# Performance work log

Hardware: AMD Instinct MI355X
Metric: run time of the kernel (lower is better)

The kernel has to match this reference:

```python
import jax, jax.numpy as jnp
import numpy as np

DIM, H, W, DEPTH = 256, 64, 64, 4
D_STATE, DT_RANK, D_CONV = 8, 16, 4
G, AGENTS = 8, 4

PKEYS = ['ln_w','ln_b','in_proj_w','conv_w','conv_b','x_proj_w','dt_proj_w','dt_proj_b',
         'A_log','A_b_log','D','out_proj_w','mn_w','mn_b']


def layernorm(x, w, b, eps=1e-5):
    mu = jnp.mean(x, -1, keepdims=True)
    var = jnp.var(x, -1, keepdims=True)
    return (x - mu) * jax.lax.rsqrt(var + eps) * w + b


def causal_conv1d(x, w, b):
    # x: (g, d, L); w: (d, k) depthwise causal conv (pad left k-1)
    k = w.shape[-1]
    xp = jnp.pad(x, ((0, 0), (0, 0), (k - 1, 0)))
    y = jax.lax.conv_general_dilated(xp, w[:, None, :], (1,), 'VALID',
                                     dimension_numbers=('NCH', 'OIH', 'NCH'),
                                     feature_group_count=w.shape[0])
    return y + b[None, :, None]


def selective_scan(u, delta, A, B, C, Dp, z):
    # u, delta, z: (g, d, L); B, C: (g, n, L); A: (d, n); Dp: (d,)
    dT = jnp.moveaxis(delta, -1, 0)
    BT = jnp.moveaxis(B, -1, 0)
    CT = jnp.moveaxis(C, -1, 0)
    uT = jnp.moveaxis(u, -1, 0)
    h0 = jnp.zeros(u.shape[:2] + (A.shape[-1],), u.dtype)  # (g, d, n)

    def step(h, inp):
        d_t, B_t, C_t, u_t = inp  # (g,d),(g,n),(g,n),(g,d)
        h = jnp.exp(d_t[..., None] * A) * h + (d_t * u_t)[..., None] * B_t[:, None, :]
        return h, jnp.einsum('gdn,gn->gd', h, C_t)

    _, ys = jax.lax.scan(step, h0, (dT, BT, CT, uT))
    y = jnp.moveaxis(ys, 0, -1) + Dp[None, :, None] * u
    return y * jax.nn.silu(z)


def ssm_dir(xdl, zdl, p, A):
    # one scan direction of mamba_inner_fn_no_out_proj; xdl, zdl: (g, d, L)
    xc = jax.nn.silu(causal_conv1d(xdl, p['conv_w'], p['conv_b']))
    x_dbl = jnp.einsum('gdl,ed->gel', xc, p['x_proj_w'])  # e = dt_rank + 2n
    dt, B, C = jnp.split(x_dbl, [DT_RANK, DT_RANK + D_STATE], axis=1)
    delta = jax.nn.softplus(jnp.einsum('grl,dr->gdl', dt, p['dt_proj_w'])
                            + p['dt_proj_b'][None, :, None])
    return selective_scan(xc, delta, A, B, C, p['D'], zdl)


def single_mamba_block(x, p):
    # x: (g, L, c)  -- LayerNorm + bidirectional Mamba (bimamba v1) + residual
    skip = x
    xn = layernorm(x, p['ln_w'], p['ln_b'])
    xz = jnp.einsum('glc,ec->gle', xn, p['in_proj_w'])  # (g, L, 2d), no bias
    xx, z = jnp.split(xz, 2, axis=-1)
    xdl = jnp.swapaxes(xx, 1, 2)
    zdl = jnp.swapaxes(z, 1, 2)
    y_f = ssm_dir(xdl, zdl, p, -jnp.exp(p['A_log']))
    y_b = jnp.flip(ssm_dir(jnp.flip(xdl, -1), jnp.flip(zdl, -1), p, -jnp.exp(p['A_b_log'])), -1)
    y = 0.5 * (y_f + y_b)  # if_devide_out=True
    out = jnp.einsum('gdl,od->glo', y, p['out_proj_w'])  # no bias
    out = layernorm(out, p['mn_w'], p['mn_b'])  # use_norm=True
    return out + skip


def _forward(data, plist, record_len):
    b, c, h, w = data.shape
    rl = np.asarray(record_len)
    seg = jnp.asarray(np.repeat(np.arange(rl.shape[0]), rl))
    means = jax.ops.segment_sum(data, seg, num_segments=rl.shape[0]) \
        / jnp.asarray(rl, data.dtype)[:, None, None, None]
    x = means.reshape(rl.shape[0], c, h * w).transpose(0, 2, 1)  # (G, L, C)
    for i in range(DEPTH):
        p = {k: v[i] for k, v in zip(PKEYS, plist)}
        x = single_mamba_block(x, p)
    return x.transpose(0, 2, 1).reshape(rl.shape[0], c, h, w)


def setup_inputs() -> dict:
    key = jax.random.key(0)
    ks = jax.random.split(key, 8)
    nrm = lambda k, shape, sc: jax.random.normal(k, shape, jnp.float32) * sc
    Alog = jnp.zeros((DEPTH, DIM, D_STATE), jnp.float32) \
        + jnp.log(jnp.arange(1, D_STATE + 1, dtype=jnp.float32))
    return {
        'data': jax.random.normal(ks[0], (G * AGENTS, DIM, H, W), jnp.float32),
        'ln_w': jnp.ones((DEPTH, DIM)), 'ln_b': jnp.zeros((DEPTH, DIM)),
        'in_proj_w': nrm(ks[1], (DEPTH, 2 * DIM, DIM), 0.02),
        'conv_w': nrm(ks[2], (DEPTH, DIM, D_CONV), 0.3),
        'conv_b': jnp.zeros((DEPTH, DIM)),
        'x_proj_w': nrm(ks[3], (DEPTH, DT_RANK + 2 * D_STATE, DIM), 0.02),
        'dt_proj_w': nrm(ks[4], (DEPTH, DIM, DT_RANK), 0.1),
        'dt_proj_b': jnp.full((DEPTH, DIM), float(np.log(np.expm1(0.01))), jnp.float32),
        'A_log': Alog, 'A_b_log': Alog,
        'D': jnp.ones((DEPTH, DIM)),
        'out_proj_w': nrm(ks[5], (DEPTH, DIM, DIM), 0.02),
        'mn_w': jnp.ones((DEPTH, DIM)), 'mn_b': jnp.zeros((DEPTH, DIM)),
        'record_len': jnp.full((G,), AGENTS, dtype=jnp.int32),
    }


def reference(data, ln_w, ln_b, in_proj_w, conv_w, conv_b, x_proj_w, dt_proj_w, dt_proj_b,
              A_log, A_b_log, D, out_proj_w, mn_w, mn_b, record_len):
    plist = [ln_w, ln_b, in_proj_w, conv_w, conv_b, x_proj_w, dt_proj_w, dt_proj_b,
             A_log, A_b_log, D, out_proj_w, mn_w, mn_b]
    return _forward(data, plist, record_len)
```

## Files before the change

### kernel.cpp

```cpp
#include <hip/hip_runtime.h>
#include <hip/hip_bf16.h>
#include <cstdint>
#include <cstddef>

typedef unsigned short u16;
typedef unsigned int   u32;

typedef short s16x8 __attribute__((ext_vector_type(8)));
typedef float f32x4 __attribute__((ext_vector_type(4)));

__device__ __forceinline__ float b2f(u16 u){ u32 x = ((u32)u)<<16; float f; __builtin_memcpy(&f,&x,4); return f; }
__device__ __forceinline__ u16  f2b(float f){ u32 x; __builtin_memcpy(&x,&f,4); u32 r = x + 0x7FFFu + ((x>>16)&1u); return (u16)(r>>16); }

__device__ __forceinline__ void unpack8(uint4 v, float* o){
  o[0]=b2f((u16)v.x); o[1]=b2f((u16)(v.x>>16));
  o[2]=b2f((u16)v.y); o[3]=b2f((u16)(v.y>>16));
  o[4]=b2f((u16)v.z); o[5]=b2f((u16)(v.z>>16));
  o[6]=b2f((u16)v.w); o[7]=b2f((u16)(v.w>>16));
}

__device__ __forceinline__ void gl_lds16(const u16* g, u16* l){
  __builtin_amdgcn_global_load_lds((const __attribute__((address_space(1))) u32*)g,
                                   (__attribute__((address_space(3))) u32*)l, 16, 0, 0);
}

__global__ void k_detect(const u16* __restrict__ lnw, int* __restrict__ flag){
  if (threadIdx.x==0 && blockIdx.x==0) *flag = (lnw[0] == 0x3F80) ? 1 : 0;
}

struct CvtTable { const void* src[14]; u16* dst[14]; int n[14]; };
__global__ void k_cvt(CvtTable t, const int* __restrict__ flag){
  int ti = blockIdx.y;
  int n = t.n[ti];
  int isbf = *flag;
  const u16*  sb = (const u16*)t.src[ti];
  const float* sf = (const float*)t.src[ti];
  u16* d = t.dst[ti];
  for (int i = blockIdx.x*256 + threadIdx.x; i < n; i += gridDim.x*256)
    d[i] = isbf ? sb[i] : f2b(sf[i]);
}

__global__ void k_mean(const void* __restrict__ data, const int* __restrict__ rl,
                       float* __restrict__ x, const int* __restrict__ flag){
  __shared__ float tile[32][129];
  int isbf = *flag;
  const u16*  db = (const u16*)data;
  const float* df_ = (const float*)data;
  int g = blockIdx.z, c0 = blockIdx.y*32, l0 = blockIdx.x*128;
  int tid = threadIdx.x;
  int off=0; for(int i=0;i<g;i++) off += rl[i];
  int cnt = rl[g];
  float inv = 1.0f/(float)cnt;
  for(int it=0; it<16; ++it){
    int idx = it*256 + tid;
    int ci = idx>>7, lj = idx&127;
    float acc = 0.f;
    for(int b=0;b<cnt;b++){
      size_t gi = ((size_t)(off+b)*256 + (c0+ci)) * 4096 + (l0+lj);
      acc += isbf ? b2f(db[gi]) : df_[gi];
    }
    tile[ci][lj] = acc*inv;
  }
  __syncthreads();
  for(int it=0; it<16; ++it){
    int idx = it*256 + tid;
    int lj = idx>>5, ci = idx&31;
    x[ ((size_t)g*4096 + (l0+lj))*256 + (c0+ci) ] = tile[ci][lj];
  }
}

__global__ void k_prep(const u16* __restrict__ dtp, const u16* __restrict__ xpw, u16* __restrict__ bcomb){
  int layer = blockIdx.y, row = blockIdx.x, c = threadIdx.x;
  u16 out;
  if (row < 256){
    float acc = 0.f;
    #pragma unroll
    for(int r=0;r<16;r++)
      acc += b2f(dtp[(size_t)layer*4096 + row*16 + r]) * b2f(xpw[(size_t)layer*8192 + r*256 + c]);
    out = f2b(acc);
  } else if (row < 272){
    out = xpw[(size_t)layer*8192 + (16 + row - 256)*256 + c];
  } else {
    out = 0;
  }
  bcomb[((size_t)layer*384 + row)*256 + c] = out;
}

__global__ void k_ln1(const float* __restrict__ x, u16* __restrict__ xn,
                      const u16* __restrict__ w, const u16* __restrict__ b, int layer){
  int wid = threadIdx.x>>6, lane = threadIdx.x&63;
  int row = blockIdx.x*4 + wid;
  const float* xr = x + (size_t)row*256;
  float4 v = *(const float4*)(xr + lane*4);
  float s = v.x+v.y+v.z+v.w;
  float q = v.x*v.x+v.y*v.y+v.z*v.z+v.w*v.w;
  for(int o=32;o;o>>=1){ s += __shfl_xor(s,o); q += __shfl_xor(q,o); }
  float mu = s*(1.f/256.f);
  float var = q*(1.f/256.f) - mu*mu;
  float rs = rsqrtf(var + 1e-5f);
  const u16* wp = w + layer*256 + lane*4;
  const u16* bp = b + layer*256 + lane*4;
  float vv[4] = {v.x,v.y,v.z,v.w};
  u16 o4[4];
  #pragma unroll
  for(int k2=0;k2<4;k2++) o4[k2] = f2b( (vv[k2]-mu)*rs*b2f(wp[k2]) + b2f(bp[k2]) );
  uint2 ov; ov.x = (u32)o4[0] | ((u32)o4[1]<<16); ov.y = (u32)o4[2] | ((u32)o4[3]<<16);
  *(uint2*)(xn + (size_t)row*256 + lane*4) = ov;
}

template<int MODE>
__global__ __launch_bounds__(256)
void k_gemm(const u16* __restrict__ A, const u16* __restrict__ B,
            u16* __restrict__ C0, int ldC,
            const u16* __restrict__ bias, u16* __restrict__ C1){
  __shared__ u16 As[128*64];
  __shared__ u16 Bs[128*64];
  int tid = threadIdx.x, wid = tid>>6, lane = tid&63;
  int m0 = blockIdx.x*128, n0 = blockIdx.y*128;
  f32x4 acc[4][4];
  #pragma unroll
  for(int i=0;i<4;i++)
    #pragma unroll
    for(int j=0;j<4;j++) acc[i][j] = (f32x4){0.f,0.f,0.f,0.f};
  int lrow  = lane>>3;
  int scol  = ((lane&7) ^ lrow) * 8;
  int rm = (wid&1)*64, cn = (wid>>1)*64;
  for(int k0=0;k0<256;k0+=64){
    #pragma unroll
    for(int it=0; it<4; ++it){
      int chunk = wid*4 + it;
      int row = chunk*8 + lrow;
      gl_lds16(A + (size_t)(m0+row)*256 + k0 + scol, As + chunk*512 + lane*8);
      gl_lds16(B + (size_t)(n0+row)*256 + k0 + scol, Bs + chunk*512 + lane*8);
    }
    __syncthreads();
    #pragma unroll
    for(int kk=0;kk<2;kk++){
      s16x8 af[4], bfr[4];
      #pragma unroll
      for(int i=0;i<4;i++){
        int ar = rm + i*16 + (lane&15);
        int ap = (kk*4 + (lane>>4)) ^ (ar&7);
        af[i]  = *(const s16x8*)(As + ar*64 + ap*8);
        int br = cn + i*16 + (lane&15);
        int bp = (kk*4 + (lane>>4)) ^ (br&7);
        bfr[i] = *(const s16x8*)(Bs + br*64 + bp*8);
      }
      #pragma unroll
      for(int i=0;i<4;i++)
        #pragma unroll
        for(int j=0;j<4;j++)
          acc[i][j] = __builtin_amdgcn_mfma_f32_16x16x32_bf16(af[i], bfr[j], acc[i][j], 0,0,0);
    }
    __syncthreads();
  }
  #pragma unroll
  for(int i=0;i<4;i++){
    #pragma unroll
    for(int j=0;j<4;j++){
      int n  = n0 + cn + j*16 + (lane&15);
      int mB = m0 + rm + i*16 + ((lane>>4)<<2);
      #pragma unroll
      for(int r=0;r<4;r++){
        float val = acc[i][j][r];
        int m = mB + r;
        if (MODE==0){
          C0[(size_t)m*ldC + n] = f2b(val);
        } else {
          if (n < 256){
            float v2 = val + b2f(bias[n]);
            float sp = (v2 > 15.f) ? v2 : __logf(1.f + __expf(v2));
            C0[(size_t)m*256 + n] = f2b(sp);
          } else if (n < 272){
            C1[(size_t)m*16 + (n-256)] = f2b(val);
          }
        }
      }
    }
  }
}

__global__ void k_conv(const u16* __restrict__ xz, const u16* __restrict__ cw,
                       const u16* __restrict__ cb, u16* __restrict__ xcf, u16* __restrict__ xcb_, int layer){
  int l0 = blockIdx.x*4, g = blockIdx.y, d = threadIdx.x;
  float w[4];
  #pragma unroll
  for(int j=0;j<4;j++) w[j] = b2f(cw[(size_t)layer*1024 + d*4 + j]);
  float bb = b2f(cb[layer*256 + d]);
  float xv[10];
  #pragma unroll
  for(int t=0;t<10;t++){
    int lp = l0 - 3 + t;
    xv[t] = (lp>=0 && lp<4096) ? b2f(xz[((size_t)g*4096 + lp)*512 + d]) : 0.f;
  }
  #pragma unroll
  for(int i=0;i<4;i++){
    float af = bb, ab = bb;
    #pragma unroll
    for(int j=0;j<4;j++){ af += w[j]*xv[i+j]; ab += w[j]*xv[i+6-j]; }
    af = af / (1.f + __expf(-af));
    ab = ab / (1.f + __expf(-ab));
    size_t o = ((size_t)g*4096 + (l0+i))*256 + d;
    xcf[o]  = f2b(af);
    xcb_[o] = f2b(ab);
  }
}

__global__ __launch_bounds__(256)
void k_scan1(const u16* __restrict__ df, const u16* __restrict__ db,
             const u16* __restrict__ uf, const u16* __restrict__ ub,
             const u16* __restrict__ bcf, const u16* __restrict__ bcb,
             const u16* __restrict__ Alog, const u16* __restrict__ Ablog,
             float* __restrict__ abuf, float* __restrict__ bbuf, int layer){
  int c = blockIdx.x, g = blockIdx.y, dir = blockIdx.z, d = threadIdx.x;
  const u16* dl = dir ? db : df;
  const u16* uu = dir ? ub : uf;
  const u16* bc = dir ? bcb : bcf;
  const u16* Al = dir ? Ablog : Alog;
  float An[8], h[8], ap[8];
  #pragma unroll
  for(int n=0;n<8;n++){
    An[n] = -__expf(b2f(Al[(size_t)layer*2048 + d*8 + n]));
    h[n] = 0.f; ap[n] = 1.f;
  }
  #pragma unroll 4
  for(int t=0;t<64;t++){
    int ts = c*64 + t;
    int tg = dir ? (4095 - ts) : ts;
    size_t rowo = (size_t)g*4096 + tg;
    float dv = b2f(dl[rowo*256 + d]);
    float uv = b2f(uu[rowo*256 + d]);
    uint4 bv = *(const uint4*)(bc + rowo*16);
    float bn[8]; unpack8(bv, bn);
    float du = dv*uv;
    #pragma unroll
    for(int n=0;n<8;n++){
      float da = __expf(dv*An[n]);
      h[n] = fmaf(da, h[n], du*bn[n]);
      ap[n] *= da;
    }
  }
  size_t base = ((((size_t)dir*8+g)*64 + c)*256 + d)*8;
  *(float4*)(abuf+base)   = (float4){ap[0],ap[1],ap[2],ap[3]};
  *(float4*)(abuf+base+4) = (float4){ap[4],ap[5],ap[6],ap[7]};
  *(float4*)(bbuf+base)   = (float4){h[0],h[1],h[2],h[3]};
  *(float4*)(bbuf+base+4) = (float4){h[4],h[5],h[6],h[7]};
}

__global__ void k_scan2(const float* __restrict__ abuf, const float* __restrict__ bbuf,
                        float* __restrict__ hs){
  int dblk = blockIdx.x, g = blockIdx.y, dir = blockIdx.z;
  int n = threadIdx.x & 7, dd = threadIdx.x >> 3;
  int d = dblk*32 + dd;
  float h = 0.f;
  size_t gofs = (((size_t)dir*8+g)*64);
  for(int c=0;c<64;c++){
    size_t idx = ((gofs + c)*256 + d)*8 + n;
    hs[idx] = h;
    h = fmaf(abuf[idx], h, bbuf[idx]);
  }
}

__global__ __launch_bounds__(256)
void k_scan3(const u16* __restrict__ df, const u16* __restrict__ db,
             const u16* __restrict__ uf, const u16* __restrict__ ub,
             const u16* __restrict__ bcf, const u16* __restrict__ bcb,
             const u16* __restrict__ Alog, const u16* __restrict__ Ablog,
             const u16* __restrict__ Dp, const u16* __restrict__ xz,
             const float* __restrict__ hs,
             u16* __restrict__ yf, u16* __restrict__ yb, int layer){
  int c = blockIdx.x, g = blockIdx.y, dir = blockIdx.z, d = threadIdx.x;
  const u16* dl = dir ? db : df;
  const u16* uu = dir ? ub : uf;
  const u16* bc = dir ? bcb : bcf;
  const u16* Al = dir ? Ablog : Alog;
  u16* yo = dir ? yb : yf;
  float An[8], h[8];
  size_t base = ((((size_t)dir*8+g)*64 + c)*256 + d)*8;
  float4 h0 = *(const float4*)(hs+base);
  float4 h1 = *(const float4*)(hs+base+4);
  h[0]=h0.x; h[1]=h0.y; h[2]=h0.z; h[3]=h0.w;
  h[4]=h1.x; h[5]=h1.y; h[6]=h1.z; h[7]=h1.w;
  #pragma unroll
  for(int n=0;n<8;n++) An[n] = -__expf(b2f(Al[(size_t)layer*2048 + d*8 + n]));
  float Dd = b2f(Dp[layer*256 + d]);
  #pragma unroll 2
  for(int t=0;t<64;t++){
    int ts = c*64 + t;
    int tg = dir ? (4095 - ts) : ts;
    size_t rowo = (size_t)g*4096 + tg;
    float dv = b2f(dl[rowo*256 + d]);
    float uv = b2f(uu[rowo*256 + d]);
    uint4 bv = *(const uint4*)(bc + rowo*16);
    uint4 cv = *(const uint4*)(bc + rowo*16 + 8);
    float bn[8], cn_[8];
    unpack8(bv, bn); unpack8(cv, cn_);
    float du = dv*uv;
    float y = 0.f;
    #pragma unroll
    for(int n=0;n<8;n++){
      float da = __expf(dv*An[n]);
      h[n] = fmaf(da, h[n], du*bn[n]);
      y = fmaf(h[n], cn_[n], y);
    }
    y += Dd*uv;
    float zv = b2f(xz[rowo*512 + 256 + d]);
    y *= zv / (1.f + __expf(-zv));
    yo[rowo*256 + d] = f2b(y);
  }
}

template<int LAST>
__global__ __launch_bounds__(256)
void k_outln(const u16* __restrict__ yf, const u16* __restrict__ yb,
             const u16* __restrict__ Bw,
             float* __restrict__ X, u16* __restrict__ xn_next,
             const u16* __restrict__ mnw, const u16* __restrict__ mnb,
             const u16* __restrict__ lnw_n, const u16* __restrict__ lnb_n){
  __shared__ u16 As[64*64];
  __shared__ u16 Bs[256*64];
  int tid = threadIdx.x, wid = tid>>6, lane = tid&63;
  int m0 = blockIdx.x*64;
  f32x4 acc[16];
  #pragma unroll
  for(int j=0;j<16;j++) acc[j] = (f32x4){0.f,0.f,0.f,0.f};
  int lrow = lane>>3;
  int scol = ((lane&7) ^ lrow) * 8;
  for(int k0=0;k0<256;k0+=64){
    #pragma unroll
    for(int s=0;s<2;s++){
      int g2 = tid + s*256;
      int row = g2>>3, p = g2&7;
      size_t off = (size_t)(m0+row)*256 + k0 + p*8;
      uint4 a = *(const uint4*)(yf + off);
      uint4 b = *(const uint4*)(yb + off);
      float fa[8], fb[8]; unpack8(a,fa); unpack8(b,fb);
      u32 o[4];
      #pragma unroll
      for(int k2=0;k2<4;k2++){
        u16 lo = f2b(0.5f*(fa[2*k2]  +fb[2*k2]));
        u16 hi = f2b(0.5f*(fa[2*k2+1]+fb[2*k2+1]));
        o[k2] = (u32)lo | ((u32)hi<<16);
      }
      *(uint4*)(As + row*64 + ((p ^ (row&7))*8)) = (uint4){o[0],o[1],o[2],o[3]};
    }
    #pragma unroll
    for(int it=0; it<8; ++it){
      int chunk = wid*8 + it;
      int row = chunk*8 + lrow;
      gl_lds16(Bw + (size_t)row*256 + k0 + scol, Bs + chunk*512 + lane*8);
    }
    __syncthreads();
    #pragma unroll
    for(int kk=0;kk<2;kk++){
      int ar = wid*16 + (lane&15);
      int ap = (kk*4 + (lane>>4)) ^ (ar&7);
      s16x8 af = *(const s16x8*)(As + ar*64 + ap*8);
      #pragma unroll
      for(int j=0;j<16;j++){
        int br = j*16 + (lane&15);
        int bp = (kk*4 + (lane>>4)) ^ (br&7);
        s16x8 bf = *(const s16x8*)(Bs + br*64 + bp*8);
        acc[j] = __builtin_amdgcn_mfma_f32_16x16x32_bf16(af, bf, acc[j], 0,0,0);
      }
    }
    __syncthreads();
  }
  int quad = lane>>4;
  float sm[4]={0,0,0,0}, sq[4]={0,0,0,0};
  #pragma unroll
  for(int j=0;j<16;j++)
    #pragma unroll
    for(int r=0;r<4;r++){ float v=acc[j][r]; sm[r]+=v; sq[r]+=v*v; }
  #pragma unroll
  for(int o=1;o<16;o<<=1)
    #pragma unroll
    for(int r=0;r<4;r++){ sm[r]+=__shfl_xor(sm[r],o); sq[r]+=__shfl_xor(sq[r],o); }
  float mu[4], rs[4];
  #pragma unroll
  for(int r=0;r<4;r++){
    mu[r] = sm[r]*(1.f/256.f);
    float var = sq[r]*(1.f/256.f) - mu[r]*mu[r];
    rs[r] = rsqrtf(var + 1e-5f);
  }
  #pragma unroll
  for(int j=0;j<16;j++){
    int col = j*16 + (lane&15);
    float w = b2f(mnw[col]), bb = b2f(mnb[col]);
    #pragma unroll
    for(int r=0;r<4;r++){
      int m = m0 + wid*16 + quad*4 + r;
      float xn = X[(size_t)m*256 + col] + (acc[j][r]-mu[r])*rs[r]*w + bb;
      X[(size_t)m*256 + col] = xn;
      acc[j][r] = xn;
    }
  }
  if (!LAST){
    float sm2[4]={0,0,0,0}, sq2[4]={0,0,0,0};
    #pragma unroll
    for(int j=0;j<16;j++)
      #pragma unroll
      for(int r=0;r<4;r++){ float v=acc[j][r]; sm2[r]+=v; sq2[r]+=v*v; }
    #pragma unroll
    for(int o=1;o<16;o<<=1)
      #pragma unroll
      for(int r=0;r<4;r++){ sm2[r]+=__shfl_xor(sm2[r],o); sq2[r]+=__shfl_xor(sq2[r],o); }
    float mu2[4], rs2[4];
    #pragma unroll
    for(int r=0;r<4;r++){
      mu2[r] = sm2[r]*(1.f/256.f);
      float var = sq2[r]*(1.f/256.f) - mu2[r]*mu2[r];
      rs2[r] = rsqrtf(var + 1e-5f);
    }
    #pragma unroll
    for(int j=0;j<16;j++){
      int col = j*16 + (lane&15);
      float w = b2f(lnw_n[col]), bb = b2f(lnb_n[col]);
      #pragma unroll
      for(int r=0;r<4;r++){
        int m = m0 + wid*16 + quad*4 + r;
        xn_next[(size_t)m*256 + col] = f2b((acc[j][r]-mu2[r])*rs2[r]*w + bb);
      }
    }
  }
}

__global__ void k_tr(const float* __restrict__ x, void* __restrict__ out, const int* __restrict__ flag){
  __shared__ float tile[32][129];
  int isbf = *flag;
  int l0 = blockIdx.x*128, c0 = blockIdx.y*32, g = blockIdx.z;
  int tid = threadIdx.x;
  for(int it=0; it<16; ++it){
    int idx = it*256 + tid;
    int lj = idx>>5, ci = idx&31;
    tile[ci][lj] = x[((size_t)g*4096 + l0+lj)*256 + c0+ci];
  }
  __syncthreads();
  for(int it=0; it<16; ++it){
    int idx = it*256 + tid;
    int lj = idx&127, ci = idx>>7;
    size_t o = ((size_t)g*256 + c0+ci)*4096 + l0+lj;
    float v = tile[ci][lj];
    if (isbf) ((u16*)out)[o] = f2b(v);
    else      ((float*)out)[o] = v;
  }
}

extern "C" void kernel_launch(void* const* d_in, const int* in_sizes, int n_in,
                              void* d_out, int out_size, void* d_ws, size_t ws_size,
                              hipStream_t stream){
  (void)in_sizes; (void)n_in; (void)out_size; (void)ws_size;
  const int* rl = (const int*)d_in[15];

  char* ws = (char*)d_ws;
  float* X    = (float*)(ws);
  u16*  XN    = (u16*)(ws + 33554432);
  u16*  XZ    = (u16*)(ws + 50331648);
  u16*  XCF   = (u16*)(ws + 83886080);
  u16*  XCB   = (u16*)(ws + 100663296);
  u16*  DF    = (u16*)(ws + 117440512);
  u16*  DB    = (u16*)(ws + 134217728);
  u16*  BCF   = (u16*)(ws + 150994944);
  u16*  BCB   = (u16*)(ws + 152043520);
  u16*  BCOMB = (u16*)(ws + 153092096);
  float* ABUF = (float*)(ws + 153878528);
  float* BBUF = (float*)(ws + 162267136);
  u16*  YF    = (u16*)(ws + 153878528);
  float* HS   = (float*)(ws + 170655744);
  u16*  YB    = (u16*)(ws + 179044352);
  u16*  WCVT  = (u16*)(ws + 195821568);
  int*  FLAG  = (int*)(ws + 197918720);

  u16* W_lnw  = WCVT + 0;
  u16* W_lnb  = WCVT + 1024;
  u16* W_inp  = WCVT + 2048;
  u16* W_cw   = WCVT + 526336;
  u16* W_cb   = WCVT + 530432;
  u16* W_xp   = WCVT + 531456;
  u16* W_dtw  = WCVT + 564224;
  u16* W_dtb  = WCVT + 580608;
  u16* W_Al   = WCVT + 581632;
  u16* W_Abl  = WCVT + 589824;
  u16* W_D    = WCVT + 598016;
  u16* W_outp = WCVT + 599040;
  u16* W_mnw  = WCVT + 861184;
  u16* W_mnb  = WCVT + 862208;

  k_detect<<<1,64,0,stream>>>((const u16*)d_in[1], FLAG);

  CvtTable t;
  const int idxs[14] = {1,2,3,4,5,6,7,8,9,10,11,12,13,14};
  u16* dsts[14] = {W_lnw,W_lnb,W_inp,W_cw,W_cb,W_xp,W_dtw,W_dtb,W_Al,W_Abl,W_D,W_outp,W_mnw,W_mnb};
  const int ns[14] = {1024,1024,524288,4096,1024,32768,16384,1024,8192,8192,1024,262144,1024,1024};
  for(int i=0;i<14;i++){ t.src[i]=d_in[idxs[i]]; t.dst[i]=dsts[i]; t.n[i]=ns[i]; }
  k_cvt<<<dim3(32,14),256,0,stream>>>(t, FLAG);

  k_mean<<<dim3(32,8,8),256,0,stream>>>(d_in[0], rl, X, FLAG);
  k_prep<<<dim3(384,4),256,0,stream>>>(W_dtw, W_xp, BCOMB);
  k_ln1<<<8192,256,0,stream>>>(X, XN, W_lnw, W_lnb, 0);

  for(int layer=0; layer<4; ++layer){
    k_gemm<0><<<dim3(256,4),256,0,stream>>>(XN, W_inp + (size_t)layer*512*256, XZ, 512, nullptr, nullptr);
    k_conv<<<dim3(1024,8),256,0,stream>>>(XZ, W_cw, W_cb, XCF, XCB, layer);
    k_gemm<1><<<dim3(512,3),256,0,stream>>>(XCF, BCOMB + (size_t)layer*384*256, DF, 256, W_dtb + layer*256, BCF);
    k_scan1<<<dim3(64,8,2),256,0,stream>>>(DF,DB,XCF,XCB,BCF,BCB,W_Al,W_Abl,ABUF,BBUF,layer);
    k_scan2<<<dim3(8,8,2),256,0,stream>>>(ABUF,BBUF,HS);
    k_scan3<<<dim3(64,8,2),256,0,stream>>>(DF,DB,XCF,XCB,BCF,BCB,W_Al,W_Abl,W_D,XZ,HS,YF,YB,layer);
    if (layer < 3){
      k_outln<0><<<512,256,0,stream>>>(YF, YB, W_outp + (size_t)layer*256*256, X, XN,
                                       W_mnw + layer*256, W_mnb + layer*256,
                                       W_lnw + (layer+1)*256, W_lnb + (layer+1)*256);
    } else {
      k_outln<1><<<512,256,0,stream>>>(YF, YB, W_outp + (size_t)layer*256*256, X, XN,
                                       W_mnw + layer*256, W_mnb + layer*256,
                                       W_lnw, W_lnb);
    }
  }
  k_tr<<<dim3(32,8,8),256,0,stream>>>(X, d_out, FLAG);
}
```

Before: 1.147 ms.

## Fuse scan output pass with out-projection GEMM and layernorm epilogue

```diff
diff --git a/kernel.cpp b/kernel.cpp
--- a/kernel.cpp
+++ b/kernel.cpp
@@ -261,66 +261,93 @@
   }
 }
 
-__global__ __launch_bounds__(256)
-void k_scan3(const u16* __restrict__ df, const u16* __restrict__ db,
-             const u16* __restrict__ uf, const u16* __restrict__ ub,
-             const u16* __restrict__ bcf, const u16* __restrict__ bcb,
-             const u16* __restrict__ Alog, const u16* __restrict__ Ablog,
-             const u16* __restrict__ Dp, const u16* __restrict__ xz,
-             const float* __restrict__ hs,
-             u16* __restrict__ yf, u16* __restrict__ yb, int layer){
-  int c = blockIdx.x, g = blockIdx.y, dir = blockIdx.z, d = threadIdx.x;
-  const u16* dl = dir ? db : df;
-  const u16* uu = dir ? ub : uf;
-  const u16* bc = dir ? bcb : bcf;
-  const u16* Al = dir ? Ablog : Alog;
-  u16* yo = dir ? yb : yf;
-  float An[8], h[8];
-  size_t base = ((((size_t)dir*8+g)*64 + c)*256 + d)*8;
-  float4 h0 = *(const float4*)(hs+base);
-  float4 h1 = *(const float4*)(hs+base+4);
-  h[0]=h0.x; h[1]=h0.y; h[2]=h0.z; h[3]=h0.w;
-  h[4]=h1.x; h[5]=h1.y; h[6]=h1.z; h[7]=h1.w;
-  #pragma unroll
-  for(int n=0;n<8;n++) An[n] = -__expf(b2f(Al[(size_t)layer*2048 + d*8 + n]));
-  float Dd = b2f(Dp[layer*256 + d]);
-  #pragma unroll 2
-  for(int t=0;t<64;t++){
-    int ts = c*64 + t;
-    int tg = dir ? (4095 - ts) : ts;
-    size_t rowo = (size_t)g*4096 + tg;
-    float dv = b2f(dl[rowo*256 + d]);
-    float uv = b2f(uu[rowo*256 + d]);
-    uint4 bv = *(const uint4*)(bc + rowo*16);
-    uint4 cv = *(const uint4*)(bc + rowo*16 + 8);
-    float bn[8], cn_[8];
-    unpack8(bv, bn); unpack8(cv, cn_);
-    float du = dv*uv;
-    float y = 0.f;
-    #pragma unroll
-    for(int n=0;n<8;n++){
-      float da = __expf(dv*An[n]);
-      h[n] = fmaf(da, h[n], du*bn[n]);
-      y = fmaf(h[n], cn_[n], y);
-    }
-    y += Dd*uv;
-    float zv = b2f(xz[rowo*512 + 256 + d]);
-    y *= zv / (1.f + __expf(-zv));
-    yo[rowo*256 + d] = f2b(y);
-  }
-}
-
+#define AP 264
 template<int LAST>
 __global__ __launch_bounds__(256)
-void k_outln(const u16* __restrict__ yf, const u16* __restrict__ yb,
-             const u16* __restrict__ Bw,
-             float* __restrict__ X, u16* __restrict__ xn_next,
-             const u16* __restrict__ mnw, const u16* __restrict__ mnb,
-             const u16* __restrict__ lnw_n, const u16* __restrict__ lnb_n){
-  __shared__ u16 As[64*64];
+void k_scanout(const u16* __restrict__ df, const u16* __restrict__ db,
+               const u16* __restrict__ uf, const u16* __restrict__ ub,
+               const u16* __restrict__ bcf, const u16* __restrict__ bcb,
+               const u16* __restrict__ Alog, const u16* __restrict__ Ablog,
+               const u16* __restrict__ Dp, const u16* __restrict__ xz,
+               const float* __restrict__ hs,
+               const u16* __restrict__ Bw,
+               float* __restrict__ X, u16* __restrict__ xn_next,
+               const u16* __restrict__ mnw, const u16* __restrict__ mnb,
+               const u16* __restrict__ lnw_n, const u16* __restrict__ lnb_n,
+               int layer){
+  __shared__ u16 As[64*AP];
   __shared__ u16 Bs[256*64];
-  int tid = threadIdx.x, wid = tid>>6, lane = tid&63;
-  int m0 = blockIdx.x*64;
+  int tid = threadIdx.x;
+  int c = blockIdx.x, g = blockIdx.y;
+  int l0 = c*64;
+  int d = tid;
+  float Dd = b2f(Dp[layer*256 + d]);
+  float An[8], h[8];
+  {
+    #pragma unroll
+    for(int n=0;n<8;n++) An[n] = -__expf(b2f(Ablog[(size_t)layer*2048 + d*8 + n]));
+    size_t base = ((((size_t)8+g)*64 + (63-c))*256 + d)*8;
+    float4 h0 = *(const float4*)(hs+base);
+    float4 h1 = *(const float4*)(hs+base+4);
+    h[0]=h0.x; h[1]=h0.y; h[2]=h0.z; h[3]=h0.w;
+    h[4]=h1.x; h[5]=h1.y; h[6]=h1.z; h[7]=h1.w;
+    #pragma unroll 2
+    for(int q=0;q<64;q++){
+      int t = 63 - q;
+      size_t rowo = (size_t)g*4096 + l0 + t;
+      float dv = b2f(db[rowo*256 + d]);
+      float uv = b2f(ub[rowo*256 + d]);
+      uint4 bv = *(const uint4*)(bcb + rowo*16);
+      uint4 cv = *(const uint4*)(bcb + rowo*16 + 8);
+      float bn[8], cn_[8];
+      unpack8(bv, bn); unpack8(cv, cn_);
+      float du = dv*uv;
+      float y = 0.f;
+      #pragma unroll
+      for(int n=0;n<8;n++){
+        float da = __expf(dv*An[n]);
+        h[n] = fmaf(da, h[n], du*bn[n]);
+        y = fmaf(h[n], cn_[n], y);
+      }
+      y += Dd*uv;
+      float zv = b2f(xz[rowo*512 + 256 + d]);
+      y *= 0.5f * zv / (1.f + __expf(-zv));
+      As[t*AP + d] = f2b(y);
+    }
+  }
+  {
+    #pragma unroll
+    for(int n=0;n<8;n++) An[n] = -__expf(b2f(Alog[(size_t)layer*2048 + d*8 + n]));
+    size_t base = (((size_t)g*64 + c)*256 + d)*8;
+    float4 h0 = *(const float4*)(hs+base);
+    float4 h1 = *(const float4*)(hs+base+4);
+    h[0]=h0.x; h[1]=h0.y; h[2]=h0.z; h[3]=h0.w;
+    h[4]=h1.x; h[5]=h1.y; h[6]=h1.z; h[7]=h1.w;
+    #pragma unroll 2
+    for(int t=0;t<64;t++){
+      size_t rowo = (size_t)g*4096 + l0 + t;
+      float dv = b2f(df[rowo*256 + d]);
+      float uv = b2f(uf[rowo*256 + d]);
+      uint4 bv = *(const uint4*)(bcf + rowo*16);
+      uint4 cv = *(const uint4*)(bcf + rowo*16 + 8);
+      float bn[8], cn_[8];
+      unpack8(bv, bn); unpack8(cv, cn_);
+      float du = dv*uv;
+      float y = 0.f;
+      #pragma unroll
+      for(int n=0;n<8;n++){
+        float da = __expf(dv*An[n]);
+        h[n] = fmaf(da, h[n], du*bn[n]);
+        y = fmaf(h[n], cn_[n], y);
+      }
+      y += Dd*uv;
+      float zv = b2f(xz[rowo*512 + 256 + d]);
+      y *= 0.5f * zv / (1.f + __expf(-zv));
+      int off = t*AP + d;
+      As[off] = f2b(b2f(As[off]) + y);
+    }
+  }
+  int wid = tid>>6, lane = tid&63;
   f32x4 acc[16];
   #pragma unroll
   for(int j=0;j<16;j++) acc[j] = (f32x4){0.f,0.f,0.f,0.f};
@@ -328,23 +355,6 @@
   int scol = ((lane&7) ^ lrow) * 8;
   for(int k0=0;k0<256;k0+=64){
     #pragma unroll
-    for(int s=0;s<2;s++){
-      int g2 = tid + s*256;
-      int row = g2>>3, p = g2&7;
-      size_t off = (size_t)(m0+row)*256 + k0 + p*8;
-      uint4 a = *(const uint4*)(yf + off);
-      uint4 b = *(const uint4*)(yb + off);
-      float fa[8], fb[8]; unpack8(a,fa); unpack8(b,fb);
-      u32 o[4];
-      #pragma unroll
-      for(int k2=0;k2<4;k2++){
-        u16 lo = f2b(0.5f*(fa[2*k2]  +fb[2*k2]));
-        u16 hi = f2b(0.5f*(fa[2*k2+1]+fb[2*k2+1]));
-        o[k2] = (u32)lo | ((u32)hi<<16);
-      }
-      *(uint4*)(As + row*64 + ((p ^ (row&7))*8)) = (uint4){o[0],o[1],o[2],o[3]};
-    }
-    #pragma unroll
     for(int it=0; it<8; ++it){
       int chunk = wid*8 + it;
       int row = chunk*8 + lrow;
@@ -354,8 +364,7 @@
     #pragma unroll
     for(int kk=0;kk<2;kk++){
       int ar = wid*16 + (lane&15);
-      int ap = (kk*4 + (lane>>4)) ^ (ar&7);
-      s16x8 af = *(const s16x8*)(As + ar*64 + ap*8);
+      s16x8 af = *(const s16x8*)(As + ar*AP + k0 + kk*32 + (lane>>4)*8);
       #pragma unroll
       for(int j=0;j<16;j++){
         int br = j*16 + (lane&15);
@@ -366,6 +375,7 @@
     }
     __syncthreads();
   }
+  size_t gm0 = (size_t)g*4096 + l0;
   int quad = lane>>4;
   float sm[4]={0,0,0,0}, sq[4]={0,0,0,0};
   #pragma unroll
@@ -389,9 +399,9 @@
     float w = b2f(mnw[col]), bb = b2f(mnb[col]);
     #pragma unroll
     for(int r=0;r<4;r++){
-      int m = m0 + wid*16 + quad*4 + r;
-      float xn = X[(size_t)m*256 + col] + (acc[j][r]-mu[r])*rs[r]*w + bb;
-      X[(size_t)m*256 + col] = xn;
+      size_t m = gm0 + wid*16 + quad*4 + r;
+      float xn = X[m*256 + col] + (acc[j][r]-mu[r])*rs[r]*w + bb;
+      X[m*256 + col] = xn;
       acc[j][r] = xn;
     }
   }
@@ -418,8 +428,8 @@
       float w = b2f(lnw_n[col]), bb = b2f(lnb_n[col]);
       #pragma unroll
       for(int r=0;r<4;r++){
-        int m = m0 + wid*16 + quad*4 + r;
-        xn_next[(size_t)m*256 + col] = f2b((acc[j][r]-mu2[r])*rs2[r]*w + bb);
+        size_t m = gm0 + wid*16 + quad*4 + r;
+        xn_next[m*256 + col] = f2b((acc[j][r]-mu2[r])*rs2[r]*w + bb);
       }
     }
   }
@@ -465,9 +475,7 @@
   u16*  BCOMB = (u16*)(ws + 153092096);
   float* ABUF = (float*)(ws + 153878528);
   float* BBUF = (float*)(ws + 162267136);
-  u16*  YF    = (u16*)(ws + 153878528);
   float* HS   = (float*)(ws + 170655744);
-  u16*  YB    = (u16*)(ws + 179044352);
   u16*  WCVT  = (u16*)(ws + 195821568);
   int*  FLAG  = (int*)(ws + 197918720);
 
@@ -505,15 +513,16 @@
     k_gemm<1><<<dim3(512,3),256,0,stream>>>(XCF, BCOMB + (size_t)layer*384*256, DF, 256, W_dtb + layer*256, BCF);
     k_scan1<<<dim3(64,8,2),256,0,stream>>>(DF,DB,XCF,XCB,BCF,BCB,W_Al,W_Abl,ABUF,BBUF,layer);
     k_scan2<<<dim3(8,8,2),256,0,stream>>>(ABUF,BBUF,HS);
-    k_scan3<<<dim3(64,8,2),256,0,stream>>>(DF,DB,XCF,XCB,BCF,BCB,W_Al,W_Abl,W_D,XZ,HS,YF,YB,layer);
     if (layer < 3){
-      k_outln<0><<<512,256,0,stream>>>(YF, YB, W_outp + (size_t)layer*256*256, X, XN,
-                                       W_mnw + layer*256, W_mnb + layer*256,
-                                       W_lnw + (layer+1)*256, W_lnb + (layer+1)*256);
+      k_scanout<0><<<dim3(64,8),256,0,stream>>>(DF,DB,XCF,XCB,BCF,BCB,W_Al,W_Abl,W_D,XZ,HS,
+                                                W_outp + (size_t)layer*256*256, X, XN,
+                                                W_mnw + layer*256, W_mnb + layer*256,
+                                                W_lnw + (layer+1)*256, W_lnb + (layer+1)*256, layer);
     } else {
-      k_outln<1><<<512,256,0,stream>>>(YF, YB, W_outp + (size_t)layer*256*256, X, XN,
-                                       W_mnw + layer*256, W_mnb + layer*256,
-                                       W_lnw, W_lnb);
+      k_scanout<1><<<dim3(64,8),256,0,stream>>>(DF,DB,XCF,XCB,BCF,BCB,W_Al,W_Abl,W_D,XZ,HS,
+                                                W_outp + (size_t)layer*256*256, X, XN,
+                                                W_mnw + layer*256, W_mnb + layer*256,
+                                                W_lnw, W_lnb, layer);
     }
   }
   k_tr<<<dim3(32,8,8),256,0,stream>>>(X, d_out, FLAG);
```

Result: no change. 1.135 ms (-1.1%).
